# Kernel tuning notes

Hardware: AMD Instinct MI355X
Metric: run time of the kernel (lower is better)

## Reference

```python
import jax, jax.numpy as jnp
import numpy as np
from jax import lax

NMS_RADIUS = 4  # module default


def conv2d(x, w, b, pad):
    # x: [B,C,H,W], w: [O,I,kh,kw]
    y = lax.conv_general_dilated(x, w, window_strides=(1, 1),
                                 padding=[(pad, pad), (pad, pad)],
                                 dimension_numbers=('NCHW', 'OIHW', 'NCHW'))
    return y + b[None, :, None, None]


def max_pool(x, r):
    # x: [B,H,W]; kernel (2r+1)x(2r+1), stride 1, pad r (torch pads with -inf)
    k = 2 * r + 1
    return lax.reduce_window(x, -jnp.inf, lax.max,
                             window_dimensions=(1, k, k),
                             window_strides=(1, 1, 1),
                             padding=[(0, 0), (r, r), (r, r)])


def simple_nms(scores, r):
    zeros = jnp.zeros_like(scores)
    max_mask = scores == max_pool(scores, r)
    for _ in range(2):
        supp_mask = max_pool(max_mask.astype(scores.dtype), r) > 0
        supp_scores = jnp.where(supp_mask, zeros, scores)
        new_max_mask = supp_scores == max_pool(supp_scores, r)
        max_mask = max_mask | (new_max_mask & ~supp_mask)
    return jnp.where(max_mask, scores, zeros)


def setup_inputs() -> dict:
    key = jax.random.key(0)
    ks = jax.random.split(key, 7)
    B, Hc, Wc = 16, 60, 80
    x = jax.random.normal(ks[0], (B, 512, Hc, Wc), dtype=jnp.float32)
    wPa = jax.random.normal(ks[1], (256, 512, 3, 3), dtype=jnp.float32) * 0.02
    bPa = jax.random.normal(ks[2], (256,), dtype=jnp.float32) * 0.02
    wPd = jax.random.normal(ks[3], (128, 256, 3, 3), dtype=jnp.float32) * 0.02
    bPd = jax.random.normal(ks[4], (128,), dtype=jnp.float32) * 0.02
    wPg = jax.random.normal(ks[5], (65, 128, 1, 1), dtype=jnp.float32) * 0.02
    bPg = jax.random.normal(ks[6], (65,), dtype=jnp.float32) * 0.02
    return {'x': x, 'wPa': wPa, 'bPa': bPa, 'wPd': wPd, 'bPd': bPd,
            'wPg': wPg, 'bPg': bPg}


def reference(x, wPa, bPa, wPd, bPd, wPg, bPg):
    h1 = jax.nn.relu(conv2d(x, wPa, bPa, pad=1))          # [B,256,Hc,Wc]
    h2 = jax.nn.relu(conv2d(h1, wPd, bPd, pad=1))         # [B,128,Hc,Wc]
    logits = conv2d(h2, wPg, bPg, pad=0)                  # [B,65,Hc,Wc]
    scores = jax.nn.softmax(logits, axis=1)[:, :-1]       # [B,64,Hc,Wc]
    b, _, h, w = scores.shape
    # pixel-unshuffle 8x8 cells -> full resolution
    scores = scores.transpose(0, 2, 3, 1).reshape(b, h, w, 8, 8)
    scores = scores.transpose(0, 1, 3, 2, 4).reshape(b, h * 8, w * 8)
    return simple_nms(scores, NMS_RADIUS)
```

## Files before the change

kernel.cpp:

```cpp
#include <hip/hip_runtime.h>
#include <hip/hip_bf16.h>
#include <math.h>


#define B_      16
#define HC      60
#define WC      80
#define PIX     (HC * WC)
#define HF      480
#define WF      640
#define IMG     (HF * WF)
#define NPIX    (B_ * IMG)

typedef double f64x4 __attribute__((ext_vector_type(4)));

__device__ __forceinline__ int clampi(int v, int lo, int hi) {
    return v < lo ? lo : (v > hi ? hi : v);
}

__global__ __launch_bounds__(256) void cvt_f32_f64(const float* __restrict__ s,
                                                   double* __restrict__ d, int n)
{
    int i = blockIdx.x * 256 + threadIdx.x;
    if (i < n) d[i] = (double)s[i];
}

__global__ __launch_bounds__(256) void prep_w(const float* __restrict__ w,
                                              double* __restrict__ wT,
                                              int CIN, int n)
{
    int i = blockIdx.x * 256 + threadIdx.x;
    if (i >= n) return;
    int cin9 = CIN * 9;
    int oc   = i / cin9;
    int rem  = i - oc * cin9;
    int ic   = rem / 9;
    int dydx = rem - ic * 9;
    size_t dst = ((size_t)((oc >> 4) * (CIN >> 2) + (ic >> 2)) * 9 + dydx) * 64
               + (ic & 3) * 16 + (oc & 15);
    wT[dst] = (double)w[i];
}

template <int CIN, typename TIN, bool RELU>
__global__ __launch_bounds__(256, 4) void conv3x3_mfma(
    const TIN* __restrict__ in,
    const double* __restrict__ wT,
    const double* __restrict__ bias,
    double* __restrict__ out)
{
    const int COUT  = (CIN == 512) ? 256 : 128;
    const int NCH   = CIN / 4;
    const int ytile = blockIdx.x;
    const int ocq   = blockIdx.y;
    const int b     = blockIdx.z;
    const int tid   = threadIdx.x;
    const int wv    = tid >> 6;
    const int lane  = tid & 63;
    const int q     = lane >> 4;
    const int c     = lane & 15;
    const int wr    = wv & 1;
    const int wo    = wv >> 1;
    const int y0    = ytile * 2;
    const int y     = y0 + wr;

    in  += (size_t)b * CIN  * PIX;
    out += (size_t)b * COUT * PIX;

    int rowL[4], colL[4];
    {
        f64x4 pr = (f64x4){0.0, 0.0, 0.0, 0.0};
        double a1 = (lane < 16) ? (double)(16 * lane) : 0.0;
        double b1 = (lane < 16) ? 1.0 : 0.0;
        pr = __builtin_amdgcn_mfma_f64_16x16x4f64(a1, b1, pr, 0, 0, 0);
        double a2 = (lane < 16) ? 1.0 : 0.0;
        double b2 = (lane < 16) ? (double)lane : 0.0;
        pr = __builtin_amdgcn_mfma_f64_16x16x4f64(a2, b2, pr, 0, 0, 0);
#pragma unroll
        for (int i = 0; i < 4; ++i) {
            int code = (int)pr[i];
            rowL[i] = (code >> 4) & 15;
            colL[i] = code & 15;
        }
    }

    __shared__ double smem[2][1312];

    const int ocb0 = ocq * 4 + wo * 2;
    const double* wA = wT + (size_t)ocb0 * NCH * 576;
    const double* wB = wT + (size_t)(ocb0 + 1) * NCH * 576;

    f64x4 acc[2][5];
#pragma unroll
    for (int o = 0; o < 2; ++o)
#pragma unroll
        for (int t = 0; t < 5; ++t) acc[o][t] = (f64x4){0.0, 0.0, 0.0, 0.0};

    const int bbase = q * 328 + wr * 82 + c;

    int aOff[6];
#pragma unroll
    for (int j = 0; j < 6; ++j) {
        int i   = tid + j * 256;
        int ick = i / 328;
        int rem = i - ick * 328;
        int ry  = rem / 82;
        int rx  = rem - ry * 82;
        int gy  = y0 - 1 + ry, gx = rx - 1;
        bool ok = (i < 1312) && ((unsigned)gy < (unsigned)HC) && ((unsigned)gx < (unsigned)WC);
        aOff[j] = ok ? (ick * PIX + gy * WC + gx) : -1;
    }

    double ra[6];

#define LOADC(ch)                                                              \
    {                                                                          \
        const int gbase = (ch) * 4 * PIX;                                      \
        _Pragma("unroll")                                                      \
        for (int j = 0; j < 6; ++j)                                            \
            ra[j] = (aOff[j] >= 0) ? (double)in[gbase + aOff[j]] : 0.0;        \
    }

#define STOREC(sel)                                                            \
    {                                                                          \
        double* dst = smem[sel];                                               \
        _Pragma("unroll")                                                      \
        for (int j = 0; j < 5; ++j) dst[tid + j * 256] = ra[j];                \
        if (tid < 32) dst[1280 + tid] = ra[5];                                 \
    }

    LOADC(0);
    STOREC(0);
    LOADC(1);
    __syncthreads();

    for (int chk = 0; chk < NCH; ++chk) {
        const int cur = chk & 1;
        if (chk + 1 < NCH) STOREC(cur ^ 1);
        if (chk + 2 < NCH) LOADC(chk + 2);

        const double* wa  = wA + (size_t)chk * 576;
        const double* wb  = wB + (size_t)chk * 576;
        const double* act = smem[cur];

#pragma unroll
        for (int dy = 0; dy < 3; ++dy) {
#pragma unroll
            for (int dx = 0; dx < 3; ++dx) {
                const int d = dy * 3 + dx;
                double a0 = wa[d * 64 + lane];
                double a1 = wb[d * 64 + lane];
#pragma unroll
                for (int t = 0; t < 5; ++t) {
                    double bv = act[bbase + dy * 82 + t * 16 + dx];
                    acc[0][t] = __builtin_amdgcn_mfma_f64_16x16x4f64(a0, bv, acc[0][t], 0, 0, 0);
                    acc[1][t] = __builtin_amdgcn_mfma_f64_16x16x4f64(a1, bv, acc[1][t], 0, 0, 0);
                }
            }
        }
        if (chk + 1 < NCH) __syncthreads();
    }
#undef LOADC
#undef STOREC

#pragma unroll
    for (int o = 0; o < 2; ++o) {
#pragma unroll
        for (int t = 0; t < 5; ++t) {
#pragma unroll
            for (int i = 0; i < 4; ++i) {
                const int oc = (ocb0 + o) * 16 + rowL[i];
                double v = acc[o][t][i] + bias[oc];
                if (RELU) v = fmax(v, 0.0);
                out[(size_t)oc * PIX + y * WC + t * 16 + colL[i]] = v;
            }
        }
    }
}

__global__ __launch_bounds__(256) void conv1x1_softmax_f64(
    const double* __restrict__ h2,
    const double* __restrict__ wg,
    const double* __restrict__ bg,
    double* __restrict__ S)
{
    int p = blockIdx.x * 256 + threadIdx.x;
    if (p >= PIX) return;
    const int b = blockIdx.y;
    const double* h2p = h2 + (size_t)b * 128 * PIX + p;
    double* Sb = S + (size_t)b * IMG;

    double l[65];
#pragma unroll
    for (int o = 0; o < 65; ++o) l[o] = bg[o];

    for (int icc = 0; icc < 128; icc += 8) {
        double h[8];
#pragma unroll
        for (int k = 0; k < 8; ++k) h[k] = h2p[(size_t)(icc + k) * PIX];
#pragma unroll
        for (int o = 0; o < 65; ++o) {
            const double* wp = wg + o * 128 + icc;
            l[o] += h[0] * wp[0] + h[1] * wp[1] + h[2] * wp[2] + h[3] * wp[3]
                  + h[4] * wp[4] + h[5] * wp[5] + h[6] * wp[6] + h[7] * wp[7];
        }
    }

    double m = l[0];
#pragma unroll
    for (int o = 1; o < 65; ++o) m = fmax(m, l[o]);
    double s = 0.0;
#pragma unroll
    for (int o = 0; o < 65; ++o) { l[o] = exp(l[o] - m); s += l[o]; }
    double inv = 1.0 / s;

    int y = p / WC, x = p % WC;
#pragma unroll
    for (int cy = 0; cy < 8; ++cy)
#pragma unroll
        for (int cx2 = 0; cx2 < 8; ++cx2)
            Sb[(y * 8 + cy) * WF + x * 8 + cx2] = l[cy * 8 + cx2] * inv;
}

__global__ __launch_bounds__(256) void hmax9_f64(const double* __restrict__ in,
                                                 double* __restrict__ out)
{
    int p = blockIdx.x * 256 + threadIdx.x;
    int x = p % WF;
    const double* row = in + (p - x);
    double m = row[x];
#pragma unroll
    for (int d = 1; d <= 4; ++d) {
        m = fmax(m, row[clampi(x - d, 0, WF - 1)]);
        m = fmax(m, row[clampi(x + d, 0, WF - 1)]);
    }
    out[p] = m;
}

__global__ __launch_bounds__(256) void vmax9_eq(const double* __restrict__ T,
                                                const double* __restrict__ S,
                                                unsigned char* __restrict__ M)
{
    int p = blockIdx.x * 256 + threadIdx.x;
    int y = (p % IMG) / WF;
    double m = T[p];
#pragma unroll
    for (int d = 1; d <= 4; ++d) {
        m = fmax(m, T[p + (clampi(y - d, 0, HF - 1) - y) * WF]);
        m = fmax(m, T[p + (clampi(y + d, 0, HF - 1) - y) * WF]);
    }
    M[p] = (S[p] == m) ? (unsigned char)1 : (unsigned char)0;
}

__global__ __launch_bounds__(256) void hor9_u8(const unsigned char* __restrict__ in,
                                               unsigned char* __restrict__ out)
{
    int p = blockIdx.x * 256 + threadIdx.x;
    int x = p % WF;
    const unsigned char* row = in + (p - x);
    unsigned char m = row[x];
#pragma unroll
    for (int d = 1; d <= 4; ++d) {
        m = m | row[clampi(x - d, 0, WF - 1)];
        m = m | row[clampi(x + d, 0, WF - 1)];
    }
    out[p] = m;
}

__global__ __launch_bounds__(256) void vor9_sup(const unsigned char* __restrict__ T8,
                                                unsigned char* __restrict__ SUP)
{
    int p = blockIdx.x * 256 + threadIdx.x;
    int y = (p % IMG) / WF;
    unsigned char m = T8[p];
#pragma unroll
    for (int d = 1; d <= 4; ++d) {
        m = m | T8[p + (clampi(y - d, 0, HF - 1) - y) * WF];
        m = m | T8[p + (clampi(y + d, 0, HF - 1) - y) * WF];
    }
    SUP[p] = m;
}

__global__ __launch_bounds__(256) void hmax9_supp(const double* __restrict__ S,
                                                  const unsigned char* __restrict__ SUP,
                                                  double* __restrict__ T)
{
    int p = blockIdx.x * 256 + threadIdx.x;
    int x = p % WF;
    int base = p - x;
    double m = SUP[p] ? 0.0 : S[p];
#pragma unroll
    for (int d = 1; d <= 4; ++d) {
        int i1 = base + clampi(x - d, 0, WF - 1);
        int i2 = base + clampi(x + d, 0, WF - 1);
        m = fmax(m, SUP[i1] ? 0.0 : S[i1]);
        m = fmax(m, SUP[i2] ? 0.0 : S[i2]);
    }
    T[p] = m;
}

__global__ __launch_bounds__(256) void vmax9_newmask(const double* __restrict__ T,
                                                     const double* __restrict__ S,
                                                     const unsigned char* __restrict__ SUP,
                                                     unsigned char* __restrict__ M)
{
    int p = blockIdx.x * 256 + threadIdx.x;
    int y = (p % IMG) / WF;
    double m = T[p];
#pragma unroll
    for (int d = 1; d <= 4; ++d) {
        m = fmax(m, T[p + (clampi(y - d, 0, HF - 1) - y) * WF]);
        m = fmax(m, T[p + (clampi(y + d, 0, HF - 1) - y) * WF]);
    }
    unsigned char nw = (!SUP[p] && S[p] == m) ? 1 : 0;
    M[p] = M[p] | nw;
}

__global__ __launch_bounds__(256) void final_mask(const double* __restrict__ S,
                                                  const unsigned char* __restrict__ M,
                                                  float* __restrict__ out)
{
    int p = blockIdx.x * 256 + threadIdx.x;
    out[p] = M[p] ? (float)S[p] : 0.f;
}

extern "C" void kernel_launch(void* const* d_in, const int* in_sizes, int n_in,
                              void* d_out, int out_size, void* d_ws, size_t ws_size,
                              hipStream_t stream)
{
    const float* x   = (const float*)d_in[0];
    const float* wPa = (const float*)d_in[1];
    const float* bPa = (const float*)d_in[2];
    const float* wPd = (const float*)d_in[3];
    const float* bPd = (const float*)d_in[4];
    const float* wPg = (const float*)d_in[5];
    const float* bPg = (const float*)d_in[6];
    float* out = (float*)d_out;

    char* ws = (char*)d_ws;
    double*        S   = (double*)(ws);
    double*        T   = (double*)(ws + 39321600);
    unsigned char* M   = (unsigned char*)(ws + 78643200);
    unsigned char* SUP = (unsigned char*)(ws + 83558400);
    unsigned char* T8  = (unsigned char*)(ws + 88473600);
    double* w1t = (double*)(ws + 39321600);
    double* w2t = (double*)(ws + 48758784);
    double* wgd = (double*)(ws + 51118080);
    double* b1d = (double*)(ws + 51184640);
    double* b2d = (double*)(ws + 51186688);
    double* bgd = (double*)(ws + 51187712);
    char*   hbase = ws + 51188736;

    int G = 1;
    for (int g = 16; g >= 1; g >>= 1) {
        if ((size_t)51188736 + (size_t)g * 14745600 <= ws_size) { G = g; break; }
    }

    prep_w<<<(1179648 + 255) / 256, 256, 0, stream>>>(wPa, w1t, 512, 1179648);
    prep_w<<<(294912 + 255) / 256, 256, 0, stream>>>(wPd, w2t, 256, 294912);
    cvt_f32_f64<<<(8320 + 255) / 256, 256, 0, stream>>>(wPg, wgd, 8320);
    cvt_f32_f64<<<1, 256, 0, stream>>>(bPa, b1d, 256);
    cvt_f32_f64<<<1, 256, 0, stream>>>(bPd, b2d, 128);
    cvt_f32_f64<<<1, 256, 0, stream>>>(bPg, bgd, 65);

    for (int bg0 = 0; bg0 < B_; bg0 += G) {
        int Gc = (bg0 + G <= B_) ? G : (B_ - bg0);
        double* h1s = (double*)hbase;
        double* h2s = (double*)(hbase + (size_t)G * 9830400);
        const float* xb = x + (size_t)bg0 * 512 * PIX;
        conv3x3_mfma<512, float, true><<<dim3(30, 4, Gc), 256, 0, stream>>>(xb, w1t, b1d, h1s);
        conv3x3_mfma<256, double, true><<<dim3(30, 2, Gc), 256, 0, stream>>>(h1s, w2t, b2d, h2s);
        conv1x1_softmax_f64<<<dim3(19, Gc), 256, 0, stream>>>(h2s, wgd, bgd, S + (size_t)bg0 * IMG);
    }

    const int NB = NPIX / 256;
    hmax9_f64<<<NB, 256, 0, stream>>>(S, T);
    vmax9_eq<<<NB, 256, 0, stream>>>(T, S, M);
    for (int it = 0; it < 2; ++it) {
        hor9_u8<<<NB, 256, 0, stream>>>(M, T8);
        vor9_sup<<<NB, 256, 0, stream>>>(T8, SUP);
        hmax9_supp<<<NB, 256, 0, stream>>>(S, SUP, T);
        vmax9_newmask<<<NB, 256, 0, stream>>>(T, S, SUP, M);
    }
    final_mask<<<NB, 256, 0, stream>>>(S, M, out);
}
```

Before: 4.384 ms.

## Triple-buffer activation staging in the conv kernel and move stores after MFMA

```diff
diff --git a/kernel.cpp b/kernel.cpp
--- a/kernel.cpp
+++ b/kernel.cpp
@@ -83,7 +83,7 @@
         }
     }
 
-    __shared__ double smem[2][1312];
+    __shared__ double smem[3][1312];
 
     const int ocb0 = ocq * 4 + wo * 2;
     const double* wA = wT + (size_t)ocb0 * NCH * 576;
@@ -128,39 +128,52 @@
         if (tid < 32) dst[1280 + tid] = ra[5];                                 \
     }
 
+#define MFMA_PHASE(br, k)                                                      \
+    {                                                                          \
+        const double* wa  = wA + (size_t)(k) * 576;                            \
+        const double* wb  = wB + (size_t)(k) * 576;                            \
+        const double* act = smem[br];                                          \
+        _Pragma("unroll")                                                      \
+        for (int dy = 0; dy < 3; ++dy) {                                       \
+            _Pragma("unroll")                                                  \
+            for (int dx = 0; dx < 3; ++dx) {                                   \
+                const int d = dy * 3 + dx;                                     \
+                double a0 = wa[d * 64 + lane];                                 \
+                double a1 = wb[d * 64 + lane];                                 \
+                _Pragma("unroll")                                              \
+                for (int t = 0; t < 5; ++t) {                                  \
+                    double bv = act[bbase + dy * 82 + t * 16 + dx];            \
+                    acc[0][t] = __builtin_amdgcn_mfma_f64_16x16x4f64(a0, bv, acc[0][t], 0, 0, 0); \
+                    acc[1][t] = __builtin_amdgcn_mfma_f64_16x16x4f64(a1, bv, acc[1][t], 0, 0, 0); \
+                }                                                              \
+            }                                                                  \
+        }                                                                      \
+    }
+
+#define CHUNK(k, br, bw)                                                       \
+    if ((k) < NCH) {                                                           \
+        const bool stage = ((k) + 2 < NCH);                                    \
+        if (stage) LOADC((k) + 2);                                             \
+        MFMA_PHASE(br, k);                                                     \
+        if (stage) STOREC(bw);                                                 \
+        if ((k) + 1 < NCH) __syncthreads();                                    \
+    }
+
     LOADC(0);
     STOREC(0);
     LOADC(1);
+    STOREC(1);
     __syncthreads();
 
-    for (int chk = 0; chk < NCH; ++chk) {
-        const int cur = chk & 1;
-        if (chk + 1 < NCH) STOREC(cur ^ 1);
-        if (chk + 2 < NCH) LOADC(chk + 2);
-
-        const double* wa  = wA + (size_t)chk * 576;
-        const double* wb  = wB + (size_t)chk * 576;
-        const double* act = smem[cur];
-
-#pragma unroll
-        for (int dy = 0; dy < 3; ++dy) {
-#pragma unroll
-            for (int dx = 0; dx < 3; ++dx) {
-                const int d = dy * 3 + dx;
-                double a0 = wa[d * 64 + lane];
-                double a1 = wb[d * 64 + lane];
-#pragma unroll
-                for (int t = 0; t < 5; ++t) {
-                    double bv = act[bbase + dy * 82 + t * 16 + dx];
-                    acc[0][t] = __builtin_amdgcn_mfma_f64_16x16x4f64(a0, bv, acc[0][t], 0, 0, 0);
-                    acc[1][t] = __builtin_amdgcn_mfma_f64_16x16x4f64(a1, bv, acc[1][t], 0, 0, 0);
-                }
-            }
-        }
-        if (chk + 1 < NCH) __syncthreads();
+    for (int chk = 0; chk < NCH; chk += 3) {
+        CHUNK(chk + 0, 0, 2);
+        CHUNK(chk + 1, 1, 0);
+        CHUNK(chk + 2, 2, 1);
     }
 #undef LOADC
 #undef STOREC
+#undef MFMA_PHASE
+#undef CHUNK
 
 #pragma unroll
     for (int o = 0; o < 2; ++o) {
```

Result: slower. 4.552 ms (+3.8%).
